# Optimization experiments

Measured on AMD Instinct MI355X. Metric: run time of the kernel, lower is better.

The kernel has to match this reference:

```python
import jax, jax.numpy as jnp
import numpy as np

N_NODES = 100000
N_EDGES = 100000
D = 768
N_TYPES = 5
LN_EPS = 1e-5


def setup_inputs() -> dict:
    key = jax.random.key(0)
    ks = jax.random.split(key, 10)
    s = 0.02
    return {
        "node_features": jax.random.normal(ks[0], (N_NODES, D), dtype=jnp.float32),
        "W_msg": jax.random.normal(ks[1], (N_TYPES, D, D), dtype=jnp.float32) * s,  # [T, out, in] (torch Linear layout)
        "b_msg": jax.random.normal(ks[2], (N_TYPES, D), dtype=jnp.float32) * s,
        "W_upd": jax.random.normal(ks[3], (D, 2 * D), dtype=jnp.float32) * s,
        "b_upd": jax.random.normal(ks[4], (D,), dtype=jnp.float32) * s,
        "ln_gamma": jnp.ones((D,), dtype=jnp.float32),
        "ln_beta": jnp.zeros((D,), dtype=jnp.float32),
        "edge_indices": jax.random.randint(ks[5], (2, N_EDGES), 0, N_NODES, dtype=jnp.int64 if jax.config.read('jax_enable_x64') else jnp.int32),
        "edge_types": jax.random.randint(ks[6], (N_EDGES,), 0, N_TYPES, dtype=jnp.int64 if jax.config.read('jax_enable_x64') else jnp.int32),
    }


def _layer_norm(x, gamma, beta):
    mu = jnp.mean(x, axis=-1, keepdims=True)
    var = jnp.var(x, axis=-1, keepdims=True)
    return (x - mu) * jax.lax.rsqrt(var + LN_EPS) * gamma + beta


def reference(node_features, W_msg, b_msg, W_upd, b_upd, ln_gamma, ln_beta, edge_indices, edge_types):
    num_nodes = node_features.shape[0]
    src, tgt = edge_indices[0], edge_indices[1]
    src_feats = node_features[src]                       # [E, D] gather

    # Per-relation-type linear message, selected by edge type mask, summed,
    # then a single scatter-add over target nodes (faithful to the torch loop).
    msgs = jnp.zeros_like(src_feats)
    for t in range(N_TYPES):
        mask = (edge_types == t).astype(src_feats.dtype)[:, None]  # [E, 1]
        m_t = src_feats @ W_msg[t].T + b_msg[t]                    # [E, D]
        msgs = msgs + m_t * mask
    aggregated = jax.ops.segment_sum(msgs, tgt, num_segments=num_nodes)  # [N, D]

    combined = jnp.concatenate([node_features, aggregated], axis=-1)     # [N, 2D]
    updated = jax.nn.relu(combined @ W_upd.T + b_upd)                    # [N, D] (dropout = eval identity)
    return _layer_norm(node_features + updated, ln_gamma, ln_beta)
```

## Files before the change

kernel.cpp:

```cpp
#include <hip/hip_runtime.h>
#include <hip/hip_bf16.h>

#define NN 100000
#define NE 100000
#define DD 768
#define NT 5

typedef __attribute__((ext_vector_type(8))) short bf16x8;
typedef __attribute__((ext_vector_type(4))) float f32x4;
typedef __attribute__((ext_vector_type(4))) unsigned short us4;

__device__ __forceinline__ unsigned short f2bf(float f) {
    unsigned int u = __builtin_bit_cast(unsigned int, f);
    u = (u + 0x7FFFu + ((u >> 16) & 1u)) >> 16;
    return (unsigned short)u;
}


__global__ void k_convw(const float* __restrict__ Wm, const float* __restrict__ Wu,
                        unsigned short* __restrict__ dst) {
    const int nm = 5 * 768 * 768 / 4, nu = 768 * 1536 / 4, n = nm + nu;
    for (int i = blockIdx.x * blockDim.x + threadIdx.x; i < n; i += gridDim.x * blockDim.x) {
        float4 v = (i < nm) ? ((const float4*)Wm)[i] : ((const float4*)Wu)[i - nm];
        us4 o = {f2bf(v.x), f2bf(v.y), f2bf(v.z), f2bf(v.w)};
        ((us4*)dst)[i] = o;
    }
}

__global__ void k_hist(const int* __restrict__ et, int* __restrict__ meta) {
    __shared__ int lc[NT];
    if (threadIdx.x < NT) lc[threadIdx.x] = 0;
    __syncthreads();
    for (int e = blockIdx.x * blockDim.x + threadIdx.x; e < NE; e += gridDim.x * blockDim.x)
        atomicAdd(&lc[et[e]], 1);
    __syncthreads();
    if (threadIdx.x < NT && lc[threadIdx.x]) atomicAdd(&meta[threadIdx.x], lc[threadIdx.x]);
}

__global__ void k_scan(int* __restrict__ meta) {
    meta[8] = 0;
    for (int t = 0; t < NT; t++) {
        int c = meta[t];
        meta[8 + t + 1] = meta[8 + t] + c;
        meta[16 + t] = meta[8 + t];
        meta[24 + t] = (c + 63) >> 6;
    }
    meta[32] = 0;
    for (int t = 0; t < NT; t++) meta[32 + t + 1] = meta[32 + t] + meta[24 + t] * 3;
}

__global__ void k_fill(const int* __restrict__ et, int* __restrict__ meta, int* __restrict__ perm) {
    __shared__ int lc[NT], gb[NT];
    if (threadIdx.x < NT) lc[threadIdx.x] = 0;
    __syncthreads();
    int e = blockIdx.x * blockDim.x + threadIdx.x;
    int t = 0, r = 0;
    if (e < NE) { t = et[e]; r = atomicAdd(&lc[t], 1); }
    __syncthreads();
    if (threadIdx.x < NT) {
        int c = lc[threadIdx.x];
        gb[threadIdx.x] = c ? atomicAdd(&meta[16 + threadIdx.x], c) : 0;
    }
    __syncthreads();
    if (e < NE) perm[gb[t] + r] = e;
}

__launch_bounds__(256)
__global__ void k_msg(const float* __restrict__ x, const unsigned short* __restrict__ WmsgB,
                      const float* __restrict__ bmsg, const int* __restrict__ esrc,
                      const int* __restrict__ etgt, const int* __restrict__ perm,
                      const int* __restrict__ meta, float* agg) {
    __shared__ unsigned short Xs[64][72];
    __shared__ unsigned short Ws[256][72];
    __shared__ int e_src[64], e_tgt[64];

    int b = blockIdx.x;
    if (b >= meta[32 + 5]) return;
    int t = 0;
    while (t < NT - 1 && b >= meta[32 + t + 1]) t++;
    int local = b - meta[32 + t];
    int ne = meta[24 + t];
    int etile = local % ne, ctile = local / ne;
    int ebase = meta[8 + t] + (etile << 6);
    int ecnt = meta[8 + t + 1] - ebase;
    if (ecnt > 64) ecnt = 64;

    int tid = threadIdx.x;
    if (tid < 64) {
        int s = 0, g = 0;
        if (tid < ecnt) { int e = perm[ebase + tid]; s = esrc[e]; g = etgt[e]; }
        e_src[tid] = s; e_tgt[tid] = g;
    }
    __syncthreads();

    int lane = tid & 63, wid = tid >> 6;
    f32x4 acc[4][4];
    #pragma unroll
    for (int m = 0; m < 4; m++)
        #pragma unroll
        for (int n = 0; n < 4; n++) acc[m][n] = (f32x4){0.f, 0.f, 0.f, 0.f};

    int row = tid >> 2, q = tid & 3;
    const unsigned short* wrow = WmsgB + (size_t)t * 768 * 768 + ((size_t)((ctile << 8) + tid)) * 768;
    int nbase = wid << 6;

    for (int kc = 0; kc < 768; kc += 64) {
        const float* xr = x + (size_t)e_src[row] * 768 + kc + (q << 4);
        #pragma unroll
        for (int j = 0; j < 4; j++) {
            float4 v = ((const float4*)xr)[j];
            us4 o = {f2bf(v.x), f2bf(v.y), f2bf(v.z), f2bf(v.w)};
            *(us4*)&Xs[row][(q << 4) + (j << 2)] = o;
        }
        #pragma unroll
        for (int j = 0; j < 8; j++) {
            uint4 v = ((const uint4*)(wrow + kc))[j];
            *(uint4*)&Ws[tid][j << 3] = v;
        }
        __syncthreads();
        #pragma unroll
        for (int ks = 0; ks < 64; ks += 32) {
            bf16x8 a[4];
            #pragma unroll
            for (int m = 0; m < 4; m++)
                a[m] = *(const bf16x8*)&Xs[(m << 4) + (lane & 15)][ks + ((lane >> 4) << 3)];
            #pragma unroll
            for (int n = 0; n < 4; n++) {
                bf16x8 bf = *(const bf16x8*)&Ws[nbase + (n << 4) + (lane & 15)][ks + ((lane >> 4) << 3)];
                #pragma unroll
                for (int m = 0; m < 4; m++)
                    acc[m][n] = __builtin_amdgcn_mfma_f32_16x16x32_bf16(a[m], bf, acc[m][n], 0, 0, 0);
            }
        }
        __syncthreads();
    }

    #pragma unroll
    for (int m = 0; m < 4; m++) {
        #pragma unroll
        for (int i = 0; i < 4; i++) {
            int r = (m << 4) + ((lane >> 4) << 2) + i;
            if (r < ecnt) {
                int tg = e_tgt[r];
                #pragma unroll
                for (int n = 0; n < 4; n++) {
                    int col = (ctile << 8) + nbase + (n << 4) + (lane & 15);
                    float v = acc[m][n][i] + bmsg[t * 768 + col];
                    unsafeAtomicAdd(&agg[(size_t)tg * 768 + col], v);
                }
            }
        }
    }
}

__launch_bounds__(512)
__global__ void k_upd(const float* __restrict__ x, const float* agg,
                      const unsigned short* __restrict__ WupdB, const float* __restrict__ bupd,
                      const float* __restrict__ gamma, const float* __restrict__ beta,
                      float* out) {
    __shared__ unsigned short Xs[64][40];
    __shared__ unsigned short Ws[768][40];
    __shared__ float red[64][2][2];

    int tid = threadIdx.x, lane = tid & 63, wid = tid >> 6;
    int wm = wid >> 1, wn = wid & 1;
    int rbase = blockIdx.x << 6;

    f32x4 acc[24];
    #pragma unroll
    for (int n = 0; n < 24; n++) acc[n] = (f32x4){0.f, 0.f, 0.f, 0.f};

    int srow = tid >> 3, sq = tid & 7;
    int grow_s = rbase + srow;
    if (grow_s >= NN) grow_s = NN - 1;

    for (int kc = 0; kc < 1536; kc += 32) {
        const float* src = (kc < 768) ? (x + (size_t)grow_s * 768 + kc)
                                      : (agg + (size_t)grow_s * 768 + (kc - 768));
        float4 v = *(const float4*)(src + (sq << 2));
        us4 o = {f2bf(v.x), f2bf(v.y), f2bf(v.z), f2bf(v.w)};
        *(us4*)&Xs[srow][sq << 2] = o;
        {
            const unsigned short* wr = WupdB + (size_t)tid * 1536 + kc;
            #pragma unroll
            for (int j = 0; j < 4; j++) *(uint4*)&Ws[tid][j << 3] = ((const uint4*)wr)[j];
            if (tid < 256) {
                const unsigned short* wr2 = WupdB + (size_t)(tid + 512) * 1536 + kc;
                #pragma unroll
                for (int j = 0; j < 4; j++) *(uint4*)&Ws[tid + 512][j << 3] = ((const uint4*)wr2)[j];
            }
        }
        __syncthreads();
        bf16x8 a = *(const bf16x8*)&Xs[(wm << 4) + (lane & 15)][(lane >> 4) << 3];
        #pragma unroll
        for (int n = 0; n < 24; n++) {
            bf16x8 bfr = *(const bf16x8*)&Ws[wn * 384 + (n << 4) + (lane & 15)][(lane >> 4) << 3];
            acc[n] = __builtin_amdgcn_mfma_f32_16x16x32_bf16(a, bfr, acc[n], 0, 0, 0);
        }
        __syncthreads();
    }

    int rl = (lane >> 4) << 2;
    float p[4] = {0, 0, 0, 0}, qq[4] = {0, 0, 0, 0};
    #pragma unroll
    for (int i = 0; i < 4; i++) {
        int grow = rbase + (wm << 4) + rl + i;
        int gr = grow < NN ? grow : NN - 1;
        #pragma unroll
        for (int n = 0; n < 24; n++) {
            int col = wn * 384 + (n << 4) + (lane & 15);
            float u = acc[n][i] + bupd[col];
            u = u > 0.f ? u : 0.f;
            float v = u + x[(size_t)gr * 768 + col];
            acc[n][i] = v;
            p[i] += v; qq[i] += v * v;
        }
    }
    #pragma unroll
    for (int i = 0; i < 4; i++) {
        #pragma unroll
        for (int m = 1; m < 16; m <<= 1) {
            p[i] += __shfl_xor(p[i], m, 64);
            qq[i] += __shfl_xor(qq[i], m, 64);
        }
    }
    if ((lane & 15) == 0) {
        #pragma unroll
        for (int i = 0; i < 4; i++) {
            int r = (wm << 4) + rl + i;
            red[r][wn][0] = p[i];
            red[r][wn][1] = qq[i];
        }
    }
    __syncthreads();
    #pragma unroll
    for (int i = 0; i < 4; i++) {
        int r = (wm << 4) + rl + i;
        int grow = rbase + r;
        if (grow < NN) {
            float s = red[r][0][0] + red[r][1][0];
            float ss = red[r][0][1] + red[r][1][1];
            float mu = s * (1.f / 768.f);
            float var = ss * (1.f / 768.f) - mu * mu;
            float rs = rsqrtf(var + 1e-5f);
            #pragma unroll
            for (int n = 0; n < 24; n++) {
                int col = wn * 384 + (n << 4) + (lane & 15);
                out[(size_t)grow * 768 + col] = (acc[n][i] - mu) * rs * gamma[col] + beta[col];
            }
        }
    }
}

extern "C" void kernel_launch(void* const* d_in, const int* in_sizes, int n_in,
                              void* d_out, int out_size, void* d_ws, size_t ws_size,
                              hipStream_t stream) {
    const float* x     = (const float*)d_in[0];
    const float* Wmsg  = (const float*)d_in[1];
    const float* bmsg  = (const float*)d_in[2];
    const float* Wupd  = (const float*)d_in[3];
    const float* bupd  = (const float*)d_in[4];
    const float* gamma = (const float*)d_in[5];
    const float* beta  = (const float*)d_in[6];
    const int* eidx    = (const int*)d_in[7];
    const int* etype   = (const int*)d_in[8];
    const int* esrc = eidx;
    const int* etgt = eidx + NE;

    unsigned short* WmsgB = (unsigned short*)d_ws;
    unsigned short* WupdB = WmsgB + 5 * 768 * 768;
    int* perm = (int*)(WupdB + 768 * 1536);
    int* meta = perm + NE;
    float* outp = (float*)d_out;

    hipMemsetAsync(d_out, 0, (size_t)NN * DD * sizeof(float), stream);
    hipMemsetAsync(meta, 0, 64 * sizeof(int), stream);
    hipLaunchKernelGGL(k_convw, dim3(2048), dim3(256), 0, stream, Wmsg, Wupd, WmsgB);
    hipLaunchKernelGGL(k_hist, dim3(256), dim3(256), 0, stream, etype, meta);
    hipLaunchKernelGGL(k_scan, dim3(1), dim3(1), 0, stream, meta);
    hipLaunchKernelGGL(k_fill, dim3((NE + 255) / 256), dim3(256), 0, stream, etype, meta, perm);
    hipLaunchKernelGGL(k_msg, dim3(4704), dim3(256), 0, stream, x, WmsgB, bmsg, esrc, etgt, perm, meta, outp);
    hipLaunchKernelGGL(k_upd, dim3((NN + 63) / 64), dim3(512), 0, stream, x, outp, WupdB, bupd, gamma, beta, outp);
}
```

Measured before the change: 2.268 ms.

## Pre-pack swizzled bf16 weights and double-buffer GEMMs with global_load_lds

Weights are pre-packed into per-32-column chunks with an XOR swizzle, so each K-chunk can be streamed straight into LDS using global_load_lds. Both GEMM kernels now double-buffer these chunks, and the fp32 activations are converted to bf16 after the LDS read. The message kernel now covers all 768 output columns per block instead of splitting them across three column tiles, so each gathered source row is loaded once rather than three times. The update kernel doubles its row tile to 128 so each weight chunk is reused across more rows. The cost is higher register and LDS pressure, and correctness now depends on hand-written vmcnt wait counts.

```diff
diff --git a/kernel.cpp b/kernel.cpp
--- a/kernel.cpp
+++ b/kernel.cpp
@@ -3,7 +3,6 @@
 
 #define NN 100000
 #define NE 100000
-#define DD 768
 #define NT 5
 
 typedef __attribute__((ext_vector_type(8))) short bf16x8;
@@ -16,14 +15,35 @@
     return (unsigned short)u;
 }
 
-
-__global__ void k_convw(const float* __restrict__ Wm, const float* __restrict__ Wu,
-                        unsigned short* __restrict__ dst) {
-    const int nm = 5 * 768 * 768 / 4, nu = 768 * 1536 / 4, n = nm + nu;
-    for (int i = blockIdx.x * blockDim.x + threadIdx.x; i < n; i += gridDim.x * blockDim.x) {
-        float4 v = (i < nm) ? ((const float4*)Wm)[i] : ((const float4*)Wu)[i - nm];
-        us4 o = {f2bf(v.x), f2bf(v.y), f2bf(v.z), f2bf(v.w)};
-        ((us4*)dst)[i] = o;
+#define GLDS16(g, l) __builtin_amdgcn_global_load_lds( \
+    (const __attribute__((address_space(1))) unsigned int*)(g), \
+    (__attribute__((address_space(3))) unsigned int*)(l), 16, 0, 0)
+
+#define BAR() do { asm volatile("" ::: "memory"); __builtin_amdgcn_s_barrier(); asm volatile("" ::: "memory"); } while (0)
+
+__global__ void k_pack(const float* __restrict__ Wm, const float* __restrict__ Wu,
+                       unsigned short* __restrict__ WmP, unsigned short* __restrict__ WuP) {
+    const int NM = 5 * 24 * 768 * 4, NU = 48 * 768 * 4;
+    for (int i = blockIdx.x * blockDim.x + threadIdx.x; i < NM + NU;
+         i += gridDim.x * blockDim.x) {
+        const float* src;
+        unsigned short* dst;
+        if (i < NM) {
+            int t = i / (24 * 768 * 4), r = i % (24 * 768 * 4);
+            int ch = r / 3072, r2 = r % 3072, n = r2 >> 2, s = r2 & 3;
+            src = Wm + ((size_t)t * 768 + n) * 768 + (ch << 5) + ((s ^ ((n >> 1) & 3)) << 3);
+            dst = WmP + (size_t)i * 8;
+        } else {
+            int j = i - NM;
+            int ch = j / 3072, r2 = j % 3072, n = r2 >> 2, s = r2 & 3;
+            src = Wu + (size_t)n * 1536 + (ch << 5) + ((s ^ ((n >> 1) & 3)) << 3);
+            dst = WuP + (size_t)j * 8;
+        }
+        float4 a = ((const float4*)src)[0], b = ((const float4*)src)[1];
+        us4 o0 = {f2bf(a.x), f2bf(a.y), f2bf(a.z), f2bf(a.w)};
+        us4 o1 = {f2bf(b.x), f2bf(b.y), f2bf(b.z), f2bf(b.w)};
+        ((us4*)dst)[0] = o0;
+        ((us4*)dst)[1] = o1;
     }
 }
 
@@ -46,7 +66,7 @@
         meta[24 + t] = (c + 63) >> 6;
     }
     meta[32] = 0;
-    for (int t = 0; t < NT; t++) meta[32 + t + 1] = meta[32 + t] + meta[24 + t] * 3;
+    for (int t = 0; t < NT; t++) meta[32 + t + 1] = meta[32 + t] + meta[24 + t];
 }
 
 __global__ void k_fill(const int* __restrict__ et, int* __restrict__ meta, int* __restrict__ perm) {
@@ -65,22 +85,20 @@
     if (e < NE) perm[gb[t] + r] = e;
 }
 
-__launch_bounds__(256)
-__global__ void k_msg(const float* __restrict__ x, const unsigned short* __restrict__ WmsgB,
+__launch_bounds__(512, 2)
+__global__ void k_msg(const float* __restrict__ x, const unsigned short* __restrict__ WmP,
                       const float* __restrict__ bmsg, const int* __restrict__ esrc,
                       const int* __restrict__ etgt, const int* __restrict__ perm,
                       const int* __restrict__ meta, float* agg) {
-    __shared__ unsigned short Xs[64][72];
-    __shared__ unsigned short Ws[256][72];
+    __shared__ __align__(16) unsigned short Ws[2][768 * 32];
+    __shared__ __align__(16) float Xs[2][64 * 32];
     __shared__ int e_src[64], e_tgt[64];
 
     int b = blockIdx.x;
-    if (b >= meta[32 + 5]) return;
+    if (b >= meta[37]) return;
     int t = 0;
     while (t < NT - 1 && b >= meta[32 + t + 1]) t++;
-    int local = b - meta[32 + t];
-    int ne = meta[24 + t];
-    int etile = local % ne, ctile = local / ne;
+    int etile = b - meta[32 + t];
     int ebase = meta[8 + t] + (etile << 6);
     int ecnt = meta[8 + t + 1] - ebase;
     if (ecnt > 64) ecnt = 64;
@@ -94,159 +112,206 @@
     __syncthreads();
 
     int lane = tid & 63, wid = tid >> 6;
-    f32x4 acc[4][4];
-    #pragma unroll
-    for (int m = 0; m < 4; m++)
-        #pragma unroll
-        for (int n = 0; n < 4; n++) acc[m][n] = (f32x4){0.f, 0.f, 0.f, 0.f};
-
-    int row = tid >> 2, q = tid & 3;
-    const unsigned short* wrow = WmsgB + (size_t)t * 768 * 768 + ((size_t)((ctile << 8) + tid)) * 768;
-    int nbase = wid << 6;
-
-    for (int kc = 0; kc < 768; kc += 64) {
-        const float* xr = x + (size_t)e_src[row] * 768 + kc + (q << 4);
-        #pragma unroll
-        for (int j = 0; j < 4; j++) {
-            float4 v = ((const float4*)xr)[j];
-            us4 o = {f2bf(v.x), f2bf(v.y), f2bf(v.z), f2bf(v.w)};
-            *(us4*)&Xs[row][(q << 4) + (j << 2)] = o;
-        }
-        #pragma unroll
-        for (int j = 0; j < 8; j++) {
-            uint4 v = ((const uint4*)(wrow + kc))[j];
-            *(uint4*)&Ws[tid][j << 3] = v;
-        }
-        __syncthreads();
-        #pragma unroll
-        for (int ks = 0; ks < 64; ks += 32) {
-            bf16x8 a[4];
-            #pragma unroll
-            for (int m = 0; m < 4; m++)
-                a[m] = *(const bf16x8*)&Xs[(m << 4) + (lane & 15)][ks + ((lane >> 4) << 3)];
-            #pragma unroll
-            for (int n = 0; n < 4; n++) {
-                bf16x8 bf = *(const bf16x8*)&Ws[nbase + (n << 4) + (lane & 15)][ks + ((lane >> 4) << 3)];
-                #pragma unroll
-                for (int m = 0; m < 4; m++)
-                    acc[m][n] = __builtin_amdgcn_mfma_f32_16x16x32_bf16(a[m], bf, acc[m][n], 0, 0, 0);
-            }
-        }
-        __syncthreads();
-    }
-
-    #pragma unroll
-    for (int m = 0; m < 4; m++) {
-        #pragma unroll
-        for (int i = 0; i < 4; i++) {
-            int r = (m << 4) + ((lane >> 4) << 2) + i;
-            if (r < ecnt) {
-                int tg = e_tgt[r];
-                #pragma unroll
-                for (int n = 0; n < 4; n++) {
-                    int col = (ctile << 8) + nbase + (n << 4) + (lane & 15);
-                    float v = acc[m][n][i] + bmsg[t * 768 + col];
-                    unsafeAtomicAdd(&agg[(size_t)tg * 768 + col], v);
-                }
-            }
-        }
-    }
-}
-
-__launch_bounds__(512)
+    int wm = wid >> 1, wn = wid & 1;
+    unsigned wave_base = tid & ~63u;
+
+    int srow = tid >> 3, sslot = tid & 7;
+    const float* xsrc_row = x + (size_t)e_src[srow] * 768 + ((sslot ^ (srow & 7)) << 2);
+    const unsigned short* wbase = WmP + (size_t)t * (24 * 768 * 32);
+
+    f32x4 acc[24];
+    #pragma unroll
+    for (int n = 0; n < 24; n++) acc[n] = (f32x4){0.f, 0.f, 0.f, 0.f};
+
+    auto stage = [&](int p, int ch) {
+        const unsigned short* wsrc = wbase + (size_t)ch * 24576;
+        #pragma unroll
+        for (int j = 0; j < 6; j++)
+            GLDS16(wsrc + ((j * 512 + tid) << 3), &Ws[p][(j * 512 + wave_base) << 3]);
+        GLDS16(xsrc_row + (ch << 5), &Xs[p][wave_base << 2]);
+    };
+
+    int g = lane >> 4;
+    int ar = (wm << 4) + (lane & 15);
+    int xoff0 = ar * 32 + ((((g << 1) + 0) ^ (ar & 7)) << 2);
+    int xoff1 = ar * 32 + ((((g << 1) + 1) ^ (ar & 7)) << 2);
+    int cn0 = wn * 384 + (lane & 15);
+
+    stage(0, 0);
+    #pragma unroll 2
+    for (int ch = 0; ch < 24; ch++) {
+        int p = ch & 1;
+        if (ch + 1 < 24) {
+            stage(p ^ 1, ch + 1);
+            asm volatile("s_waitcnt vmcnt(7)" ::: "memory");
+        } else {
+            asm volatile("s_waitcnt vmcnt(0)" ::: "memory");
+        }
+        BAR();
+        f32x4 fa0 = *(const f32x4*)&Xs[p][xoff0];
+        f32x4 fa1 = *(const f32x4*)&Xs[p][xoff1];
+        bf16x8 a;
+        a[0] = (short)f2bf(fa0[0]); a[1] = (short)f2bf(fa0[1]);
+        a[2] = (short)f2bf(fa0[2]); a[3] = (short)f2bf(fa0[3]);
+        a[4] = (short)f2bf(fa1[0]); a[5] = (short)f2bf(fa1[1]);
+        a[6] = (short)f2bf(fa1[2]); a[7] = (short)f2bf(fa1[3]);
+        #pragma unroll
+        for (int nf = 0; nf < 24; nf++) {
+            int n = cn0 + (nf << 4);
+            bf16x8 bb = *(const bf16x8*)&Ws[p][(n << 5) + ((g ^ ((n >> 1) & 3)) << 3)];
+            acc[nf] = __builtin_amdgcn_mfma_f32_16x16x32_bf16(a, bb, acc[nf], 0, 0, 0);
+        }
+        BAR();
+    }
+
+    const float* bms = bmsg + t * 768;
+    int g4 = (lane >> 4) << 2;
+    #pragma unroll
+    for (int i = 0; i < 4; i++) {
+        int r = (wm << 4) + g4 + i;
+        bool ok = r < ecnt;
+        int tg = e_tgt[r];
+        #pragma unroll
+        for (int nf = 0; nf < 24; nf++) {
+            int col = cn0 + (nf << 4);
+            float v = acc[nf][i] + bms[col];
+            if (ok) unsafeAtomicAdd(&agg[(size_t)tg * 768 + col], v);
+        }
+    }
+}
+
+__launch_bounds__(512, 2)
 __global__ void k_upd(const float* __restrict__ x, const float* agg,
-                      const unsigned short* __restrict__ WupdB, const float* __restrict__ bupd,
+                      const unsigned short* __restrict__ WuP, const float* __restrict__ bupd,
                       const float* __restrict__ gamma, const float* __restrict__ beta,
                       float* out) {
-    __shared__ unsigned short Xs[64][40];
-    __shared__ unsigned short Ws[768][40];
-    __shared__ float red[64][2][2];
+    __shared__ __align__(16) unsigned short Ws[2][768 * 32];
+    __shared__ __align__(16) float Xs[2][128 * 32];
+    __shared__ float red[128][4];
 
     int tid = threadIdx.x, lane = tid & 63, wid = tid >> 6;
     int wm = wid >> 1, wn = wid & 1;
-    int rbase = blockIdx.x << 6;
-
-    f32x4 acc[24];
-    #pragma unroll
-    for (int n = 0; n < 24; n++) acc[n] = (f32x4){0.f, 0.f, 0.f, 0.f};
-
-    int srow = tid >> 3, sq = tid & 7;
-    int grow_s = rbase + srow;
-    if (grow_s >= NN) grow_s = NN - 1;
-
-    for (int kc = 0; kc < 1536; kc += 32) {
-        const float* src = (kc < 768) ? (x + (size_t)grow_s * 768 + kc)
-                                      : (agg + (size_t)grow_s * 768 + (kc - 768));
-        float4 v = *(const float4*)(src + (sq << 2));
-        us4 o = {f2bf(v.x), f2bf(v.y), f2bf(v.z), f2bf(v.w)};
-        *(us4*)&Xs[srow][sq << 2] = o;
+    int rbase = blockIdx.x << 7;
+    unsigned wave_base = tid & ~63u;
+
+    int r0 = tid >> 3, s0 = tid & 7;
+    int r1 = (tid + 512) >> 3;
+    int rg0 = rbase + r0; if (rg0 >= NN) rg0 = NN - 1;
+    int rg1 = rbase + r1; if (rg1 >= NN) rg1 = NN - 1;
+    size_t xo0 = (size_t)rg0 * 768 + ((s0 ^ (r0 & 7)) << 2);
+    size_t xo1 = (size_t)rg1 * 768 + ((s0 ^ (r1 & 7)) << 2);
+
+    f32x4 acc[2][24];
+    #pragma unroll
+    for (int m = 0; m < 2; m++)
+        #pragma unroll
+        for (int n = 0; n < 24; n++) acc[m][n] = (f32x4){0.f, 0.f, 0.f, 0.f};
+
+    auto stage = [&](int p, int ch) {
+        const unsigned short* wsrc = WuP + (size_t)ch * 24576;
+        #pragma unroll
+        for (int j = 0; j < 6; j++)
+            GLDS16(wsrc + ((j * 512 + tid) << 3), &Ws[p][(j * 512 + wave_base) << 3]);
+        int kc = ch << 5;
+        const float* f0 = (kc < 768) ? (x + xo0 + kc) : (agg + xo0 + (kc - 768));
+        const float* f1 = (kc < 768) ? (x + xo1 + kc) : (agg + xo1 + (kc - 768));
+        GLDS16(f0, &Xs[p][wave_base << 2]);
+        GLDS16(f1, &Xs[p][(512 + wave_base) << 2]);
+    };
+
+    int g = lane >> 4;
+    int ar0 = (wm << 5) + (lane & 15);
+    int xoffA[2][2];
+    #pragma unroll
+    for (int m = 0; m < 2; m++) {
+        int ar = ar0 + (m << 4);
+        xoffA[m][0] = ar * 32 + ((((g << 1) + 0) ^ (ar & 7)) << 2);
+        xoffA[m][1] = ar * 32 + ((((g << 1) + 1) ^ (ar & 7)) << 2);
+    }
+    int cn0 = wn * 384 + (lane & 15);
+
+    stage(0, 0);
+    #pragma unroll 2
+    for (int ch = 0; ch < 48; ch++) {
+        int p = ch & 1;
+        if (ch + 1 < 48) {
+            stage(p ^ 1, ch + 1);
+            asm volatile("s_waitcnt vmcnt(8)" ::: "memory");
+        } else {
+            asm volatile("s_waitcnt vmcnt(0)" ::: "memory");
+        }
+        BAR();
+        bf16x8 a0, a1;
         {
-            const unsigned short* wr = WupdB + (size_t)tid * 1536 + kc;
+            f32x4 f00 = *(const f32x4*)&Xs[p][xoffA[0][0]];
+            f32x4 f01 = *(const f32x4*)&Xs[p][xoffA[0][1]];
+            f32x4 f10 = *(const f32x4*)&Xs[p][xoffA[1][0]];
+            f32x4 f11 = *(const f32x4*)&Xs[p][xoffA[1][1]];
+            a0[0] = (short)f2bf(f00[0]); a0[1] = (short)f2bf(f00[1]);
+            a0[2] = (short)f2bf(f00[2]); a0[3] = (short)f2bf(f00[3]);
+            a0[4] = (short)f2bf(f01[0]); a0[5] = (short)f2bf(f01[1]);
+            a0[6] = (short)f2bf(f01[2]); a0[7] = (short)f2bf(f01[3]);
+            a1[0] = (short)f2bf(f10[0]); a1[1] = (short)f2bf(f10[1]);
+            a1[2] = (short)f2bf(f10[2]); a1[3] = (short)f2bf(f10[3]);
+            a1[4] = (short)f2bf(f11[0]); a1[5] = (short)f2bf(f11[1]);
+            a1[6] = (short)f2bf(f11[2]); a1[7] = (short)f2bf(f11[3]);
+        }
+        #pragma unroll
+        for (int nf = 0; nf < 24; nf++) {
+            int n = cn0 + (nf << 4);
+            bf16x8 bb = *(const bf16x8*)&Ws[p][(n << 5) + ((g ^ ((n >> 1) & 3)) << 3)];
+            acc[0][nf] = __builtin_amdgcn_mfma_f32_16x16x32_bf16(a0, bb, acc[0][nf], 0, 0, 0);
+            acc[1][nf] = __builtin_amdgcn_mfma_f32_16x16x32_bf16(a1, bb, acc[1][nf], 0, 0, 0);
+        }
+        BAR();
+    }
+
+    int g4 = (lane >> 4) << 2;
+    #pragma unroll
+    for (int m = 0; m < 2; m++) {
+        #pragma unroll
+        for (int i = 0; i < 4; i++) {
+            int r = (wm << 5) + (m << 4) + g4 + i;
+            int grow = rbase + r;
+            int gr = grow < NN ? grow : NN - 1;
+            const float* xr = x + (size_t)gr * 768;
+            float a_ = 0.f, b_ = 0.f;
             #pragma unroll
-            for (int j = 0; j < 4; j++) *(uint4*)&Ws[tid][j << 3] = ((const uint4*)wr)[j];
-            if (tid < 256) {
-                const unsigned short* wr2 = WupdB + (size_t)(tid + 512) * 1536 + kc;
+            for (int nf = 0; nf < 24; nf++) {
+                int col = cn0 + (nf << 4);
+                float u = acc[m][nf][i] + bupd[col];
+                u = u > 0.f ? u : 0.f;
+                float v = u + xr[col];
+                acc[m][nf][i] = v;
+                a_ += v; b_ += v * v;
+            }
+            #pragma unroll
+            for (int d = 1; d < 16; d <<= 1) {
+                a_ += __shfl_xor(a_, d, 64);
+                b_ += __shfl_xor(b_, d, 64);
+            }
+            if ((lane & 15) == 0) { red[r][wn * 2] = a_; red[r][wn * 2 + 1] = b_; }
+        }
+    }
+    __syncthreads();
+    #pragma unroll
+    for (int m = 0; m < 2; m++) {
+        #pragma unroll
+        for (int i = 0; i < 4; i++) {
+            int r = (wm << 5) + (m << 4) + g4 + i;
+            int grow = rbase + r;
+            if (grow < NN) {
+                float s = red[r][0] + red[r][2];
+                float ss = red[r][1] + red[r][3];
+                float mu = s * (1.f / 768.f);
+                float var = ss * (1.f / 768.f) - mu * mu;
+                float rs = rsqrtf(var + 1e-5f);
+                float* orow = out + (size_t)grow * 768;
                 #pragma unroll
-                for (int j = 0; j < 4; j++) *(uint4*)&Ws[tid + 512][j << 3] = ((const uint4*)wr2)[j];
-            }
-        }
-        __syncthreads();
-        bf16x8 a = *(const bf16x8*)&Xs[(wm << 4) + (lane & 15)][(lane >> 4) << 3];
-        #pragma unroll
-        for (int n = 0; n < 24; n++) {
-            bf16x8 bfr = *(const bf16x8*)&Ws[wn * 384 + (n << 4) + (lane & 15)][(lane >> 4) << 3];
-            acc[n] = __builtin_amdgcn_mfma_f32_16x16x32_bf16(a, bfr, acc[n], 0, 0, 0);
-        }
-        __syncthreads();
-    }
-
-    int rl = (lane >> 4) << 2;
-    float p[4] = {0, 0, 0, 0}, qq[4] = {0, 0, 0, 0};
-    #pragma unroll
-    for (int i = 0; i < 4; i++) {
-        int grow = rbase + (wm << 4) + rl + i;
-        int gr = grow < NN ? grow : NN - 1;
-        #pragma unroll
-        for (int n = 0; n < 24; n++) {
-            int col = wn * 384 + (n << 4) + (lane & 15);
-            float u = acc[n][i] + bupd[col];
-            u = u > 0.f ? u : 0.f;
-            float v = u + x[(size_t)gr * 768 + col];
-            acc[n][i] = v;
-            p[i] += v; qq[i] += v * v;
-        }
-    }
-    #pragma unroll
-    for (int i = 0; i < 4; i++) {
-        #pragma unroll
-        for (int m = 1; m < 16; m <<= 1) {
-            p[i] += __shfl_xor(p[i], m, 64);
-            qq[i] += __shfl_xor(qq[i], m, 64);
-        }
-    }
-    if ((lane & 15) == 0) {
-        #pragma unroll
-        for (int i = 0; i < 4; i++) {
-            int r = (wm << 4) + rl + i;
-            red[r][wn][0] = p[i];
-            red[r][wn][1] = qq[i];
-        }
-    }
-    __syncthreads();
-    #pragma unroll
-    for (int i = 0; i < 4; i++) {
-        int r = (wm << 4) + rl + i;
-        int grow = rbase + r;
-        if (grow < NN) {
-            float s = red[r][0][0] + red[r][1][0];
-            float ss = red[r][0][1] + red[r][1][1];
-            float mu = s * (1.f / 768.f);
-            float var = ss * (1.f / 768.f) - mu * mu;
-            float rs = rsqrtf(var + 1e-5f);
-            #pragma unroll
-            for (int n = 0; n < 24; n++) {
-                int col = wn * 384 + (n << 4) + (lane & 15);
-                out[(size_t)grow * 768 + col] = (acc[n][i] - mu) * rs * gamma[col] + beta[col];
+                for (int nf = 0; nf < 24; nf++) {
+                    int col = cn0 + (nf << 4);
+                    orow[col] = (acc[m][nf][i] - mu) * rs * gamma[col] + beta[col];
+                }
             }
         }
     }
@@ -267,18 +332,18 @@
     const int* esrc = eidx;
     const int* etgt = eidx + NE;
 
-    unsigned short* WmsgB = (unsigned short*)d_ws;
-    unsigned short* WupdB = WmsgB + 5 * 768 * 768;
-    int* perm = (int*)(WupdB + 768 * 1536);
+    unsigned short* WmP = (unsigned short*)d_ws;
+    unsigned short* WuP = WmP + (size_t)5 * 24 * 768 * 32;
+    int* perm = (int*)(WuP + (size_t)48 * 768 * 32);
     int* meta = perm + NE;
     float* outp = (float*)d_out;
 
-    hipMemsetAsync(d_out, 0, (size_t)NN * DD * sizeof(float), stream);
+    hipMemsetAsync(d_out, 0, (size_t)NN * 768 * sizeof(float), stream);
     hipMemsetAsync(meta, 0, 64 * sizeof(int), stream);
-    hipLaunchKernelGGL(k_convw, dim3(2048), dim3(256), 0, stream, Wmsg, Wupd, WmsgB);
+    hipLaunchKernelGGL(k_pack, dim3(1024), dim3(256), 0, stream, Wmsg, Wupd, WmP, WuP);
     hipLaunchKernelGGL(k_hist, dim3(256), dim3(256), 0, stream, etype, meta);
     hipLaunchKernelGGL(k_scan, dim3(1), dim3(1), 0, stream, meta);
     hipLaunchKernelGGL(k_fill, dim3((NE + 255) / 256), dim3(256), 0, stream, etype, meta, perm);
-    hipLaunchKernelGGL(k_msg, dim3(4704), dim3(256), 0, stream, x, WmsgB, bmsg, esrc, etgt, perm, meta, outp);
-    hipLaunchKernelGGL(k_upd, dim3((NN + 63) / 64), dim3(512), 0, stream, x, outp, WupdB, bupd, gamma, beta, outp);
-}
+    hipLaunchKernelGGL(k_msg, dim3(1568), dim3(512), 0, stream, x, WmP, bmsg, esrc, etgt, perm, meta, outp);
+    hipLaunchKernelGGL(k_upd, dim3((NN + 127) / 128), dim3(512), 0, stream, x, outp, WuP, bupd, gamma, beta, outp);
+}
```

After: 1.850 ms. 1.23x faster.
